# Optimization experiments

Measured on AMD Instinct MI355X. Metric: run time of the kernel, lower is better.

The kernel has to match this reference:

```python
import jax, jax.numpy as jnp
import numpy as np

EMBED = 1024
HEADS = 16
HEAD_DIM = EMBED // HEADS
HIDDEN = int(EMBED * 4.0)
EPS = 1e-6


def setup_inputs() -> dict:
    key = jax.random.key(0)
    ks = jax.random.split(key, 8)
    s = lambda fan_in: 1.0 / np.sqrt(fan_in)
    x = jax.random.normal(ks[0], (2, 2048, EMBED), dtype=jnp.float32)
    return {
        "x": x,
        "ln1_g": jnp.ones((EMBED,), jnp.float32),
        "ln1_b": jnp.zeros((EMBED,), jnp.float32),
        "w_qkv": jax.random.normal(ks[1], (EMBED, 3 * EMBED), jnp.float32) * s(EMBED),
        "b_qkv": jnp.zeros((3 * EMBED,), jnp.float32),
        "w_proj": jax.random.normal(ks[2], (EMBED, EMBED), jnp.float32) * s(EMBED),
        "b_proj": jnp.zeros((EMBED,), jnp.float32),
        "ln2_g": jnp.ones((EMBED,), jnp.float32),
        "ln2_b": jnp.zeros((EMBED,), jnp.float32),
        "w_fc1": jax.random.normal(ks[3], (EMBED, HIDDEN), jnp.float32) * s(EMBED),
        "b_fc1": jnp.zeros((HIDDEN,), jnp.float32),
        "w_fc2": jax.random.normal(ks[4], (HIDDEN, EMBED), jnp.float32) * s(HIDDEN),
        "b_fc2": jnp.zeros((EMBED,), jnp.float32),
    }


def _layernorm(x, g, b):
    mu = jnp.mean(x, axis=-1, keepdims=True)
    var = jnp.mean(jnp.square(x - mu), axis=-1, keepdims=True)
    return (x - mu) * jax.lax.rsqrt(var + EPS) * g + b


def _attention(x, w_qkv, b_qkv, w_proj, b_proj):
    B, N, C = x.shape
    qkv = x @ w_qkv + b_qkv                      # [B,N,3C]
    qkv = qkv.reshape(B, N, 3, HEADS, HEAD_DIM)
    q, k, v = (qkv[:, :, 0], qkv[:, :, 1], qkv[:, :, 2])  # [B,N,H,Dh]
    scale = HEAD_DIM ** -0.5
    attn = jnp.einsum('bnhd,bmhd->bhnm', q, k) * scale     # [B,H,N,N]
    attn = jax.nn.softmax(attn, axis=-1)
    out = jnp.einsum('bhnm,bmhd->bnhd', attn, v).reshape(B, N, C)
    return out @ w_proj + b_proj


def reference(x, ln1_g, ln1_b, w_qkv, b_qkv, w_proj, b_proj,
              ln2_g, ln2_b, w_fc1, b_fc1, w_fc2, b_fc2):
    x = x + _attention(_layernorm(x, ln1_g, ln1_b), w_qkv, b_qkv, w_proj, b_proj)
    h = _layernorm(x, ln2_g, ln2_b)
    h = jax.nn.gelu(h @ w_fc1 + b_fc1, approximate=False)
    x = x + (h @ w_fc2 + b_fc2)
    return x
```

## Files before the change

### kernel.cpp

```cpp
#include <hip/hip_runtime.h>
#include <hip/hip_bf16.h>
#include <math.h>

typedef __bf16 bf16x8 __attribute__((ext_vector_type(8)));
typedef __bf16 bf16x4 __attribute__((ext_vector_type(4)));
typedef unsigned short u16x8 __attribute__((ext_vector_type(8)));
typedef float f32x4 __attribute__((ext_vector_type(4)));

#define EP_QKV 0
#define EP_GELU 1
#define EP_RES 2

static __device__ __forceinline__ unsigned short f2bf(float x) {
  unsigned int u = __float_as_uint(x);
  unsigned int r = (u + 0x7fffu + ((u >> 16) & 1u)) >> 16;
  return (unsigned short)r;
}

static __device__ __forceinline__ unsigned int pkbf(float lo, float hi) {
  return __builtin_amdgcn_perm(__float_as_uint(hi), __float_as_uint(lo), 0x07060302);
}

static __device__ __forceinline__ void async16(const void* g, void* l) {
  __builtin_amdgcn_global_load_lds((__attribute__((address_space(1))) void*)g,
                                   (__attribute__((address_space(3))) void*)l, 16, 0, 0);
}

__global__ __launch_bounds__(256) void wt_all(
    const float* __restrict__ i0, unsigned short* __restrict__ o0,
    const float* __restrict__ i1, unsigned short* __restrict__ o1,
    const float* __restrict__ i2, unsigned short* __restrict__ o2,
    const float* __restrict__ i3, unsigned short* __restrict__ o3) {
  __shared__ float tile[32][33];
  const int b = blockIdx.x;
  const float* in; unsigned short* out; int K, N, nbx, lb;
  if (b < 3072)      { in = i0; out = o0; K = 1024; N = 3072; nbx = 96;  lb = b; }
  else if (b < 4096) { in = i1; out = o1; K = 1024; N = 1024; nbx = 32;  lb = b - 3072; }
  else if (b < 8192) { in = i2; out = o2; K = 1024; N = 4096; nbx = 128; lb = b - 4096; }
  else               { in = i3; out = o3; K = 4096; N = 1024; nbx = 32;  lb = b - 8192; }
  const int n0 = (lb % nbx) * 32;
  const int k0 = (lb / nbx) * 32;
  const int tx = threadIdx.x;
  const int ty = threadIdx.y;
  #pragma unroll
  for (int i = ty; i < 32; i += 8)
    tile[i][tx] = in[(size_t)(k0 + i) * N + n0 + tx];
  __syncthreads();
  #pragma unroll
  for (int i = ty; i < 32; i += 8)
    out[(size_t)(n0 + i) * K + k0 + tx] = f2bf(tile[tx][i]);
}

__global__ __launch_bounds__(256) void ln_kernel(const float* __restrict__ x,
                                                 const float* __restrict__ g,
                                                 const float* __restrict__ b,
                                                 unsigned short* __restrict__ outp) {
  const int row = blockIdx.x;
  const int tid = threadIdx.x;
  const int wave = tid >> 6, lane = tid & 63;
  const float4 v = ((const float4*)(x + (size_t)row * 1024))[tid];
  float s = v.x + v.y + v.z + v.w;
  #pragma unroll
  for (int i = 1; i < 64; i <<= 1) s += __shfl_xor(s, i);
  __shared__ float red[4];
  if (lane == 0) red[wave] = s;
  __syncthreads();
  const float mean = (red[0] + red[1] + red[2] + red[3]) * (1.f / 1024.f);
  const float dx = v.x - mean, dy = v.y - mean, dz = v.z - mean, dw = v.w - mean;
  float ss = dx * dx + dy * dy + dz * dz + dw * dw;
  #pragma unroll
  for (int i = 1; i < 64; i <<= 1) ss += __shfl_xor(ss, i);
  __syncthreads();
  if (lane == 0) red[wave] = ss;
  __syncthreads();
  const float var = (red[0] + red[1] + red[2] + red[3]) * (1.f / 1024.f);
  const float inv = rsqrtf(var + 1e-6f);
  const float4 gv = ((const float4*)g)[tid];
  const float4 bv = ((const float4*)b)[tid];
  ushort4 o;
  o.x = f2bf(dx * inv * gv.x + bv.x);
  o.y = f2bf(dy * inv * gv.y + bv.y);
  o.z = f2bf(dz * inv * gv.z + bv.z);
  o.w = f2bf(dw * inv * gv.w + bv.w);
  ((ushort4*)(outp + (size_t)row * 1024))[tid] = o;
}

template <int TN, int BK, bool DBUF, int MODE, int MINW>
__global__ __launch_bounds__(256, MINW) void gemm_kernel(
    const unsigned short* __restrict__ A,
    const unsigned short* __restrict__ BT,
    const float* __restrict__ bias,
    int M, int N, int K,
    void* __restrict__ outp, const float* __restrict__ res) {
  constexpr int AM = (TN == 128) ? 4 : 2;
  constexpr int ACH = BK / 16;
  constexpr int BCH = TN * BK / 2048;
  constexpr int CPR = BK / 8;
  constexpr int ABYTES = 256 * BK;
  constexpr int BBYTES = TN * BK * 2;
  constexpr int NBUF = DBUF ? 2 : 1;
  __shared__ __align__(16) char smem[NBUF * (ABYTES + BBYTES)];

  const int tid = threadIdx.x;
  const int wave = tid >> 6, lane = tid & 63;
  const int quad = lane >> 4, l16 = lane & 15;
  const int wm = (TN == 128) ? (wave >> 1) : wave;
  const int wn = (TN == 128) ? (wave & 1) : 0;

  const int nbm = M >> 7, nbn = N / TN;
  const int lin = blockIdx.y * gridDim.x + blockIdx.x;
  const int g = lin & 7, idx = lin >> 3;
  const int gm = nbm >> 2, gn = nbn >> 1;
  const int bm = (g & 3) * gm + (idx % gm);
  const int bn = (g >> 2) * gn + (idx / gm);
  const int row_m = bm * 128, row_n = bn * TN;

  int ar[ACH], ac[ACH];
  #pragma unroll
  for (int i = 0; i < ACH; ++i) {
    const int c = wave * (64 * ACH) + i * 64 + lane;
    ar[i] = c / CPR;
    ac[i] = ((c % CPR) ^ (ar[i] & (CPR - 1))) * 8;
  }
  int br[BCH], bc[BCH];
  #pragma unroll
  for (int i = 0; i < BCH; ++i) {
    const int c = wave * (64 * BCH) + i * 64 + lane;
    br[i] = c / CPR;
    bc[i] = ((c % CPR) ^ (br[i] & (CPR - 1))) * 8;
  }

  const unsigned short* Ag = A + (size_t)row_m * K;
  const unsigned short* Bg = BT + (size_t)row_n * K;

  const f32x4 z = {0.f, 0.f, 0.f, 0.f};
  f32x4 acc[AM][4];
  #pragma unroll
  for (int i = 0; i < AM; ++i)
    #pragma unroll
    for (int j = 0; j < 4; ++j) acc[i][j] = z;

  auto issue = [&](int kt, int b) {
    unsigned short* As = (unsigned short*)(smem + b * ABYTES);
    unsigned short* Bs = (unsigned short*)(smem + NBUF * ABYTES + b * BBYTES);
    #pragma unroll
    for (int i = 0; i < ACH; ++i)
      async16(Ag + (size_t)ar[i] * K + kt + ac[i], As + wave * (ACH * 512) + i * 512);
    #pragma unroll
    for (int i = 0; i < BCH; ++i)
      async16(Bg + (size_t)br[i] * K + kt + bc[i], Bs + wave * (BCH * 512) + i * 512);
  };

  auto computeTile = [&](int b) {
    const unsigned short* As = (const unsigned short*)(smem + b * ABYTES);
    const unsigned short* Bs = (const unsigned short*)(smem + NBUF * ABYTES + b * BBYTES);
    #pragma unroll
    for (int h = 0; h < BK / 32; ++h) {
      bf16x8 af[AM], bfv[4];
      #pragma unroll
      for (int t = 0; t < AM; ++t) {
        const int row = wm * (AM * 16) + t * 16 + l16;
        const int ch = (h * 4 + quad) ^ (row & (CPR - 1));
        af[t] = *(const bf16x8*)(As + row * BK + ch * 8);
      }
      #pragma unroll
      for (int t = 0; t < 4; ++t) {
        const int row = wn * 64 + t * 16 + l16;
        const int ch = (h * 4 + quad) ^ (row & (CPR - 1));
        bfv[t] = *(const bf16x8*)(Bs + row * BK + ch * 8);
      }
      #pragma unroll
      for (int tm = 0; tm < AM; ++tm)
        #pragma unroll
        for (int tn = 0; tn < 4; ++tn)
          acc[tm][tn] = __builtin_amdgcn_mfma_f32_16x16x32_bf16(af[tm], bfv[tn], acc[tm][tn], 0, 0, 0);
    }
  };

  if constexpr (DBUF) {
    issue(0, 0);
    for (int kt = 0; kt < K; kt += BK) {
      const int b = (kt / BK) & 1;
      __syncthreads();
      if (kt + BK < K) issue(kt + BK, b ^ 1);
      computeTile(b);
    }
  } else {
    for (int kt = 0; kt < K; kt += BK) {
      issue(kt, 0);
      __syncthreads();
      computeTile(0);
      __syncthreads();
    }
  }

  #pragma unroll
  for (int tn = 0; tn < 4; ++tn) {
    const int col = row_n + wn * 64 + tn * 16 + l16;
    const float bv = bias[col];
    #pragma unroll
    for (int tm = 0; tm < AM; ++tm) {
      const int rbase = row_m + wm * (AM * 16) + tm * 16 + quad * 4;
      float v[4];
      #pragma unroll
      for (int r = 0; r < 4; ++r) v[r] = acc[tm][tn][r] + bv;
      if constexpr (MODE == EP_QKV) {
        unsigned short* outw = (unsigned short*)outp;
        const int which = col >> 10;
        const int h = (col >> 6) & 15, d = col & 63;
        const int bb = rbase >> 11, n = rbase & 2047;
        const size_t bh = (size_t)(bb * 16 + h);
        if (which == 0) {
          #pragma unroll
          for (int r = 0; r < 4; ++r)
            outw[(bh * 2048 + n + r) * 64 + d] = f2bf(v[r] * 0.18033688011112043f);
        } else if (which == 1) {
          #pragma unroll
          for (int r = 0; r < 4; ++r)
            outw[4194304ull + (bh * 2048 + n + r) * 64 + d] = f2bf(v[r]);
        } else {
          uint2 o;
          o.x = pkbf(v[0], v[1]);
          o.y = pkbf(v[2], v[3]);
          *(uint2*)(outw + 8388608ull + (bh * 64 + d) * 2048 + n) = o;
        }
      } else if constexpr (MODE == EP_GELU) {
        #pragma unroll
        for (int r = 0; r < 4; ++r) {
          const float u = v[r];
          const float c = 1.5957691216f * fmaf(0.044715f * u * u, u, u);
          const float e = __expf(c);
          const float gl = u - __fdividef(u, e + 1.0f);
          ((unsigned short*)outp)[(size_t)(rbase + r) * N + col] = f2bf(gl);
        }
      } else {
        #pragma unroll
        for (int r = 0; r < 4; ++r)
          ((float*)outp)[(size_t)(rbase + r) * N + col] =
              res[(size_t)(rbase + r) * N + col] + v[r];
      }
    }
  }
}

template <int MODE>
__global__ __launch_bounds__(512, 2) void gemm256_kernel(
    const unsigned short* __restrict__ A,
    const unsigned short* __restrict__ BT,
    const float* __restrict__ bias,
    int M, int N, int K,
    void* __restrict__ outp, const float* __restrict__ res) {
  __shared__ __align__(16) char smem[131072];

  const int tid = threadIdx.x;
  const int wave = tid >> 6, lane = tid & 63;
  const int quad = lane >> 4, l16 = lane & 15;
  const int wm = wave >> 2;
  const int wn = wave & 3;

  const int nbm = M >> 8, nbn = N >> 8;
  const int lin = blockIdx.y * gridDim.x + blockIdx.x;
  const int g = lin & 7, idx = lin >> 3;
  const int gm = nbm >> 2, gn = nbn >> 1;
  const int bm = (g & 3) * gm + (idx % gm);
  const int bn = (g >> 2) * gn + (idx / gm);
  const int row_m = bm * 256, row_n = bn * 256;

  int ar[4], ac[4];
  #pragma unroll
  for (int i = 0; i < 4; ++i) {
    const int c = wave * 256 + i * 64 + lane;
    const int rr = c >> 3;
    ar[i] = rr;
    ac[i] = ((c & 7) ^ (rr & 7)) * 8;
  }

  const unsigned short* Ag = A + (size_t)row_m * K;
  const unsigned short* Bg = BT + (size_t)row_n * K;

  const f32x4 z = {0.f, 0.f, 0.f, 0.f};
  f32x4 acc[8][4];
  #pragma unroll
  for (int i = 0; i < 8; ++i)
    #pragma unroll
    for (int j = 0; j < 4; ++j) acc[i][j] = z;

  auto issue = [&](int kt, int b) {
    unsigned short* As = (unsigned short*)(smem + b * 65536);
    unsigned short* Bs = (unsigned short*)(smem + b * 65536 + 32768);
    #pragma unroll
    for (int i = 0; i < 4; ++i)
      async16(Ag + (size_t)ar[i] * K + kt + ac[i], As + wave * 2048 + i * 512);
    #pragma unroll
    for (int i = 0; i < 4; ++i)
      async16(Bg + (size_t)ar[i] * K + kt + ac[i], Bs + wave * 2048 + i * 512);
  };

  auto computeTile = [&](int b) {
    const unsigned short* As = (const unsigned short*)(smem + b * 65536);
    const unsigned short* Bs = (const unsigned short*)(smem + b * 65536 + 32768);
    #pragma unroll
    for (int h = 0; h < 2; ++h) {
      bf16x8 bfv[4];
      #pragma unroll
      for (int t = 0; t < 4; ++t) {
        const int row = wn * 64 + t * 16 + l16;
        const int ch = (h * 4 + quad) ^ (row & 7);
        bfv[t] = *(const bf16x8*)(Bs + row * 64 + ch * 8);
      }
      #pragma unroll
      for (int tm = 0; tm < 8; ++tm) {
        const int row = wm * 128 + tm * 16 + l16;
        const int ch = (h * 4 + quad) ^ (row & 7);
        bf16x8 af = *(const bf16x8*)(As + row * 64 + ch * 8);
        #pragma unroll
        for (int tn = 0; tn < 4; ++tn)
          acc[tm][tn] = __builtin_amdgcn_mfma_f32_16x16x32_bf16(af, bfv[tn], acc[tm][tn], 0, 0, 0);
      }
    }
  };

  issue(0, 0);
  for (int t = 0; t < 16; ++t) {
    const int b = t & 1;
    issue((t + 1) * 64, b ^ 1);
    asm volatile("s_waitcnt vmcnt(8) lgkmcnt(0)\n\ts_barrier" ::: "memory");
    computeTile(b);
    asm volatile("s_waitcnt lgkmcnt(0)\n\ts_barrier" ::: "memory");
  }

  #pragma unroll
  for (int tn = 0; tn < 4; ++tn) {
    const int col = row_n + wn * 64 + tn * 16 + l16;
    const float bv = bias[col];
    #pragma unroll
    for (int tm = 0; tm < 8; ++tm) {
      const int rbase = row_m + wm * 128 + tm * 16 + quad * 4;
      float v[4];
      #pragma unroll
      for (int r = 0; r < 4; ++r) v[r] = acc[tm][tn][r] + bv;
      if constexpr (MODE == EP_GELU) {
        #pragma unroll
        for (int r = 0; r < 4; ++r) {
          const float u = v[r];
          const float c = 1.5957691216f * fmaf(0.044715f * u * u, u, u);
          const float e = __expf(c);
          const float gl = u - __fdividef(u, e + 1.0f);
          ((unsigned short*)outp)[(size_t)(rbase + r) * N + col] = f2bf(gl);
        }
      } else {
        #pragma unroll
        for (int r = 0; r < 4; ++r)
          ((float*)outp)[(size_t)(rbase + r) * N + col] =
              res[(size_t)(rbase + r) * N + col] + v[r];
      }
    }
  }
}

__global__ __launch_bounds__(256, 3) void attn_kernel(
    const unsigned short* __restrict__ Q,
    const unsigned short* __restrict__ Kb,
    const unsigned short* __restrict__ VT,
    unsigned short* __restrict__ outp) {
  __shared__ __align__(16) char smem[49152];
  unsigned short* Ks = (unsigned short*)smem;
  unsigned short* Vs = (unsigned short*)(smem + 32768);

  const int tid = threadIdx.x;
  const int wave = tid >> 6, lane = tid & 63;
  const int quad = lane >> 4, l16 = lane & 15;

  const int lin = blockIdx.y * gridDim.x + blockIdx.x;
  const int g = lin & 7, idx = lin >> 3;
  const int bhi = g * 4 + (idx >> 5);
  const int q0 = (idx & 31) * 64;

  const unsigned short* Qg = Q + ((size_t)bhi * 2048 + q0) * 64;
  const unsigned short* Kg = Kb + (size_t)bhi * 2048 * 64;
  const unsigned short* Vg = VT + (size_t)bhi * 64 * 2048;

  const unsigned short* kp[4];
  const unsigned short* vp[4];
  #pragma unroll
  for (int i = 0; i < 4; ++i) {
    const int c = wave * 256 + i * 64 + lane;
    const int krr = c >> 3, kcc = ((c & 7) ^ (krr & 7)) * 8;
    const int vrr = c >> 4, vcc = ((c & 15) ^ (vrr & 15)) * 8;
    kp[i] = Kg + (size_t)krr * 64 + kcc;
    vp[i] = Vg + (size_t)vrr * 2048 + vcc;
  }

  auto issueK = [&](int b) {
    unsigned short* Kd = Ks + b * 8192;
    #pragma unroll
    for (int i = 0; i < 4; ++i) async16(kp[i], Kd + wave * 2048 + i * 512);
    #pragma unroll
    for (int i = 0; i < 4; ++i) kp[i] += 8192;
  };
  auto issueV = [&]() {
    #pragma unroll
    for (int i = 0; i < 4; ++i) async16(vp[i], Vs + wave * 2048 + i * 512);
    #pragma unroll
    for (int i = 0; i < 4; ++i) vp[i] += 128;
  };

  issueK(0);

  bf16x8 qb[4][2];
  #pragma unroll
  for (int nt = 0; nt < 4; ++nt)
    #pragma unroll
    for (int h = 0; h < 2; ++h)
      qb[nt][h] = *(const bf16x8*)(Qg + (nt * 16 + l16) * 64 + (h * 4 + quad) * 8);

  const f32x4 z = {0.f, 0.f, 0.f, 0.f};
  f32x4 acc[4][4];
  #pragma unroll
  for (int i = 0; i < 4; ++i)
    #pragma unroll
    for (int j = 0; j < 4; ++j) acc[i][j] = z;
  float lsum[4] = {0.f, 0.f, 0.f, 0.f};

  const int rowA = wave * 16 + l16;
  const int rowB = 64 + rowA;
  const int swk = l16 & 7;

  bf16x8 pb[4];
  auto computeQK = [&](int b) {
    const unsigned short* Ksb = Ks + b * 8192;
    f32x4 sA[4], sB[4];
    #pragma unroll
    for (int nt = 0; nt < 4; ++nt) { sA[nt] = z; sB[nt] = z; }
    __builtin_amdgcn_s_setprio(1);
    #pragma unroll
    for (int h = 0; h < 2; ++h) {
      const int ch = (h * 4 + quad) ^ swk;
      bf16x8 kfA = *(const bf16x8*)(Ksb + rowA * 64 + ch * 8);
      bf16x8 kfB = *(const bf16x8*)(Ksb + rowB * 64 + ch * 8);
      #pragma unroll
      for (int nt = 0; nt < 4; ++nt) {
        sA[nt] = __builtin_amdgcn_mfma_f32_16x16x32_bf16(kfA, qb[nt][h], sA[nt], 0, 0, 0);
        sB[nt] = __builtin_amdgcn_mfma_f32_16x16x32_bf16(kfB, qb[nt][h], sB[nt], 0, 0, 0);
      }
    }
    __builtin_amdgcn_s_setprio(0);
    #pragma unroll
    for (int nt = 0; nt < 4; ++nt) {
      union { unsigned int d[4]; bf16x8 b; } cv;
      float pa[4], pv[4];
      float ls = 0.f;
      #pragma unroll
      for (int r = 0; r < 4; ++r) {
        pa[r] = __builtin_amdgcn_exp2f(sA[nt][r]);
        pv[r] = __builtin_amdgcn_exp2f(sB[nt][r]);
        ls += pa[r] + pv[r];
      }
      cv.d[0] = pkbf(pa[0], pa[1]);
      cv.d[1] = pkbf(pa[2], pa[3]);
      cv.d[2] = pkbf(pv[0], pv[1]);
      cv.d[3] = pkbf(pv[2], pv[3]);
      lsum[nt] += ls;
      pb[nt] = cv.b;
    }
  };

  auto computePV = [&]() {
    __builtin_amdgcn_s_setprio(1);
    #pragma unroll
    for (int mt = 0; mt < 4; ++mt) {
      const int d = mt * 16 + l16;
      const int cA = (wave * 2 + (quad >> 1)) ^ (d & 15);
      const int cB = (8 + wave * 2 + (quad >> 1)) ^ (d & 15);
      const int sub = (quad & 1) * 4;
      bf16x4 vA = *(const bf16x4*)(Vs + d * 128 + cA * 8 + sub);
      bf16x4 vB = *(const bf16x4*)(Vs + d * 128 + cB * 8 + sub);
      bf16x8 vf = __builtin_shufflevector(vA, vB, 0, 1, 2, 3, 4, 5, 6, 7);
      #pragma unroll
      for (int nt = 0; nt < 4; ++nt)
        acc[mt][nt] = __builtin_amdgcn_mfma_f32_16x16x32_bf16(vf, pb[nt], acc[mt][nt], 0, 0, 0);
    }
    __builtin_amdgcn_s_setprio(0);
  };

  for (int t = 0; t < 16; ++t) {
    __syncthreads();
    issueV();
    issueK((t + 1) & 1);
    computeQK(t & 1);
    asm volatile("s_waitcnt vmcnt(4) lgkmcnt(0)\n\ts_barrier" ::: "memory");
    computePV();
  }
  __syncthreads();

  float* sc = (float*)smem;
  float* lred = (float*)(smem + 32768);
  #pragma unroll
  for (int nt = 0; nt < 4; ++nt) {
    float ls = lsum[nt];
    ls += __shfl_xor(ls, 16);
    ls += __shfl_xor(ls, 32);
    if (quad == 0) lred[wave * 64 + nt * 16 + l16] = ls;
  }
  if (wave >= 2) {
    float* dst = sc + (wave - 2) * 4096;
    #pragma unroll
    for (int mt = 0; mt < 4; ++mt)
      #pragma unroll
      for (int nt = 0; nt < 4; ++nt)
        *(f32x4*)(dst + (mt * 4 + nt) * 256 + lane * 4) = acc[mt][nt];
  }
  __syncthreads();
  if (wave < 2) {
    const float* src = sc + wave * 4096;
    #pragma unroll
    for (int mt = 0; mt < 4; ++mt)
      #pragma unroll
      for (int nt = 0; nt < 4; ++nt)
        acc[mt][nt] += *(const f32x4*)(src + (mt * 4 + nt) * 256 + lane * 4);
  }
  if (wave == 1) {
    float* dst = sc + 4096;
    #pragma unroll
    for (int mt = 0; mt < 4; ++mt)
      #pragma unroll
      for (int nt = 0; nt < 4; ++nt)
        *(f32x4*)(dst + (mt * 4 + nt) * 256 + lane * 4) = acc[mt][nt];
  }
  __syncthreads();
  if (wave == 0) {
    const float* src = sc + 4096;
    float linv[4];
    #pragma unroll
    for (int nt = 0; nt < 4; ++nt) {
      const int qi = nt * 16 + l16;
      const float l = lred[qi] + lred[64 + qi] + lred[128 + qi] + lred[192 + qi];
      linv[nt] = 1.0f / l;
    }
    const int b = bhi >> 4, h = bhi & 15;
    #pragma unroll
    for (int mt = 0; mt < 4; ++mt)
      #pragma unroll
      for (int nt = 0; nt < 4; ++nt) {
        f32x4 o = acc[mt][nt] + *(const f32x4*)(src + (mt * 4 + nt) * 256 + lane * 4);
        uint2 ov;
        ov.x = pkbf(o[0] * linv[nt], o[1] * linv[nt]);
        ov.y = pkbf(o[2] * linv[nt], o[3] * linv[nt]);
        *(uint2*)(outp + ((size_t)(b * 2048 + q0 + nt * 16 + l16)) * 1024 +
                  h * 64 + mt * 16 + quad * 4) = ov;
      }
  }
}

extern "C" void kernel_launch(void* const* d_in, const int* in_sizes, int n_in,
                              void* d_out, int out_size, void* d_ws, size_t ws_size,
                              hipStream_t stream) {
  (void)in_sizes; (void)n_in; (void)out_size; (void)ws_size;
  const float* x      = (const float*)d_in[0];
  const float* ln1_g  = (const float*)d_in[1];
  const float* ln1_b  = (const float*)d_in[2];
  const float* w_qkv  = (const float*)d_in[3];
  const float* b_qkv  = (const float*)d_in[4];
  const float* w_proj = (const float*)d_in[5];
  const float* b_proj = (const float*)d_in[6];
  const float* ln2_g  = (const float*)d_in[7];
  const float* ln2_b  = (const float*)d_in[8];
  const float* w_fc1  = (const float*)d_in[9];
  const float* b_fc1  = (const float*)d_in[10];
  const float* w_fc2  = (const float*)d_in[11];
  const float* b_fc2  = (const float*)d_in[12];

  char* ws = (char*)d_ws;
  unsigned short* wqkvT  = (unsigned short*)(ws + 0);
  unsigned short* wprojT = (unsigned short*)(ws + 6291456);
  unsigned short* wfc1T  = (unsigned short*)(ws + 8388608);
  unsigned short* wfc2T  = (unsigned short*)(ws + 16777216);
  unsigned short* lnb    = (unsigned short*)(ws + 25165824);
  unsigned short* qkvb   = (unsigned short*)(ws + 33554432);
  unsigned short* attnb  = (unsigned short*)(ws + 58720256);
  float*          x2     = (float*)(ws + 67108864);
  unsigned short* hbuf   = qkvb;

  wt_all<<<12288, dim3(32, 8), 0, stream>>>(w_qkv, wqkvT, w_proj, wprojT,
                                            w_fc1, wfc1T, w_fc2, wfc2T);

  ln_kernel<<<4096, 256, 0, stream>>>(x, ln1_g, ln1_b, lnb);

  gemm_kernel<128, 64, false, EP_QKV, 3><<<dim3(24, 32), 256, 0, stream>>>(
      lnb, wqkvT, b_qkv, 4096, 3072, 1024, (void*)qkvb, nullptr);

  attn_kernel<<<dim3(32, 32), 256, 0, stream>>>(qkvb, qkvb + 4194304, qkvb + 8388608, attnb);

  gemm_kernel<64, 64, true, EP_RES, 2><<<dim3(16, 32), 256, 0, stream>>>(
      attnb, wprojT, b_proj, 4096, 1024, 1024, (void*)x2, x);

  ln_kernel<<<4096, 256, 0, stream>>>(x2, ln2_g, ln2_b, lnb);

  gemm256_kernel<EP_GELU><<<dim3(16, 16), 512, 0, stream>>>(
      lnb, wfc1T, b_fc1, 4096, 4096, 1024, (void*)hbuf, nullptr);

  gemm_kernel<64, 64, true, EP_RES, 2><<<dim3(16, 32), 256, 0, stream>>>(
      hbuf, wfc2T, b_fc2, 4096, 1024, 4096, d_out, x2);
}
```

Before: 319.0 us.

## Interleave half-tile async staging with MFMA phases in the GEMM main loop

Replaces the per-iteration issue-all-then-compute GEMM loop with a four-phase schedule. Each K step is split into MFMA halves. B for the next step is staged in halves between those phases, and A is prefetched two steps ahead into the buffer just consumed. s_setprio is raised around MFMA bursts. The goal is to hide global-to-LDS latency and LDS read stalls behind matrix work, at the cost of more barriers per iteration and prefetches that read past K on the final iterations.

```diff
diff --git a/kernel.cpp b/kernel.cpp
--- a/kernel.cpp
+++ b/kernel.cpp
@@ -266,15 +266,6 @@
   const int bn = (g >> 2) * gn + (idx / gm);
   const int row_m = bm * 256, row_n = bn * 256;
 
-  int ar[4], ac[4];
-  #pragma unroll
-  for (int i = 0; i < 4; ++i) {
-    const int c = wave * 256 + i * 64 + lane;
-    const int rr = c >> 3;
-    ar[i] = rr;
-    ac[i] = ((c & 7) ^ (rr & 7)) * 8;
-  }
-
   const unsigned short* Ag = A + (size_t)row_m * K;
   const unsigned short* Bg = BT + (size_t)row_n * K;
 
@@ -285,60 +276,101 @@
     #pragma unroll
     for (int j = 0; j < 4; ++j) acc[i][j] = z;
 
-  auto issue = [&](int kt, int b) {
-    unsigned short* As = (unsigned short*)(smem + b * 65536);
-    unsigned short* Bs = (unsigned short*)(smem + b * 65536 + 32768);
-    #pragma unroll
-    for (int i = 0; i < 4; ++i)
-      async16(Ag + (size_t)ar[i] * K + kt + ac[i], As + wave * 2048 + i * 512);
-    #pragma unroll
-    for (int i = 0; i < 4; ++i)
-      async16(Bg + (size_t)ar[i] * K + kt + ac[i], Bs + wave * 2048 + i * 512);
-  };
-
-  auto computeTile = [&](int b) {
+  auto stageHalfA = [&](int kt, int bufb, int H) {
+    unsigned short* dst = (unsigned short*)(smem + bufb * 65536) + H * 8192;
+    const unsigned short* src = Ag + (size_t)H * 128 * K + kt;
+    #pragma unroll
+    for (int i = 0; i < 2; ++i) {
+      const int c = i * 512 + tid;
+      const int rr = c >> 3, cc = ((c & 7) ^ (rr & 7)) * 8;
+      async16(src + (size_t)rr * K + cc, dst + c * 8);
+    }
+  };
+  auto stageHalfB = [&](int kt, int bufb, int H) {
+    unsigned short* dst = (unsigned short*)(smem + bufb * 65536) + 16384 + H * 8192;
+    const unsigned short* src = Bg + (size_t)H * 128 * K + kt;
+    #pragma unroll
+    for (int i = 0; i < 2; ++i) {
+      const int c = i * 512 + tid;
+      const int rr = c >> 3, cc = ((c & 7) ^ (rr & 7)) * 8;
+      async16(src + (size_t)rr * K + cc, dst + c * 8);
+    }
+  };
+
+  stageHalfA(0, 0, 0);  stageHalfA(0, 0, 1);
+  stageHalfB(0, 0, 0);  stageHalfB(0, 0, 1);
+  stageHalfA(64, 1, 0); stageHalfA(64, 1, 1);
+  asm volatile("s_waitcnt vmcnt(4)" ::: "memory");
+  __builtin_amdgcn_s_barrier();
+
+  for (int t = 0; t < 16; ++t) {
+    const int b = t & 1;
     const unsigned short* As = (const unsigned short*)(smem + b * 65536);
-    const unsigned short* Bs = (const unsigned short*)(smem + b * 65536 + 32768);
-    #pragma unroll
-    for (int h = 0; h < 2; ++h) {
-      bf16x8 bfv[4];
-      #pragma unroll
-      for (int t = 0; t < 4; ++t) {
-        const int row = wn * 64 + t * 16 + l16;
-        const int ch = (h * 4 + quad) ^ (row & 7);
-        bfv[t] = *(const bf16x8*)(Bs + row * 64 + ch * 8);
-      }
+    const unsigned short* Bs = As + 16384;
+    const int kt1 = (t + 1) * 64, kt2 = (t + 2) * 64;
+
+    bf16x8 af[8], bv[2];
+
+    auto readA = [&](int h) {
       #pragma unroll
       for (int tm = 0; tm < 8; ++tm) {
         const int row = wm * 128 + tm * 16 + l16;
         const int ch = (h * 4 + quad) ^ (row & 7);
-        bf16x8 af = *(const bf16x8*)(As + row * 64 + ch * 8);
+        af[tm] = *(const bf16x8*)(As + row * 64 + ch * 8);
+      }
+    };
+    auto readB2 = [&](int h, int p) {
+      #pragma unroll
+      for (int j = 0; j < 2; ++j) {
+        const int row = wn * 64 + (p * 2 + j) * 16 + l16;
+        const int ch = (h * 4 + quad) ^ (row & 7);
+        bv[j] = *(const bf16x8*)(Bs + row * 64 + ch * 8);
+      }
+    };
+    auto mfma16 = [&](int p) {
+      __builtin_amdgcn_s_setprio(1);
+      #pragma unroll
+      for (int tm = 0; tm < 8; ++tm)
         #pragma unroll
-        for (int tn = 0; tn < 4; ++tn)
-          acc[tm][tn] = __builtin_amdgcn_mfma_f32_16x16x32_bf16(af, bfv[tn], acc[tm][tn], 0, 0, 0);
-      }
-    }
-  };
-
-  issue(0, 0);
-  for (int t = 0; t < 16; ++t) {
-    const int b = t & 1;
-    issue((t + 1) * 64, b ^ 1);
-    asm volatile("s_waitcnt vmcnt(8) lgkmcnt(0)\n\ts_barrier" ::: "memory");
-    computeTile(b);
-    asm volatile("s_waitcnt lgkmcnt(0)\n\ts_barrier" ::: "memory");
+        for (int j = 0; j < 2; ++j)
+          acc[tm][p * 2 + j] =
+              __builtin_amdgcn_mfma_f32_16x16x32_bf16(af[tm], bv[j], acc[tm][p * 2 + j], 0, 0, 0);
+      __builtin_amdgcn_s_setprio(0);
+    };
+
+    readA(0); readB2(0, 0);
+    stageHalfB(kt1, b ^ 1, 0);
+    __builtin_amdgcn_s_barrier();
+    mfma16(0);
+    __builtin_amdgcn_s_barrier();
+    readB2(0, 1);
+    stageHalfB(kt1, b ^ 1, 1);
+    __builtin_amdgcn_s_barrier();
+    mfma16(1);
+    __builtin_amdgcn_s_barrier();
+    readA(1); readB2(1, 0);
+    __builtin_amdgcn_s_barrier();
+    mfma16(0);
+    __builtin_amdgcn_s_barrier();
+    readB2(1, 1);
+    stageHalfA(kt2, b, 0);
+    stageHalfA(kt2, b, 1);
+    __builtin_amdgcn_s_barrier();
+    mfma16(1);
+    asm volatile("s_waitcnt vmcnt(4)" ::: "memory");
+    __builtin_amdgcn_s_barrier();
   }
 
   #pragma unroll
   for (int tn = 0; tn < 4; ++tn) {
     const int col = row_n + wn * 64 + tn * 16 + l16;
-    const float bv = bias[col];
+    const float bvb = bias[col];
     #pragma unroll
     for (int tm = 0; tm < 8; ++tm) {
       const int rbase = row_m + wm * 128 + tm * 16 + quad * 4;
       float v[4];
       #pragma unroll
-      for (int r = 0; r < 4; ++r) v[r] = acc[tm][tn][r] + bv;
+      for (int r = 0; r < 4; ++r) v[r] = acc[tm][tn][r] + bvb;
       if constexpr (MODE == EP_GELU) {
         #pragma unroll
         for (int r = 0; r < 4; ++r) {
```

Result: slower. 331.2 us (+3.8%).
